# Optimization experiments

Hardware: AMD Instinct MI355X
Metric: run time of the kernel (lower is better)

The kernel has to match this reference:

```python
import jax, jax.numpy as jnp
import numpy as np

N = 50000
NEG_SLOPE = 0.2


def add_self_loops(edge_index, n):
    loop = jnp.arange(n, dtype=edge_index.dtype)
    return jnp.concatenate([edge_index, jnp.stack([loop, loop])], axis=1)


def gatv2_conv(x, edge_index, Wl, bl, Wr, br, att, bias):
    """PyG GATv2Conv (share_weights=False, concat=True, add_self_loops applied by caller).
    x: [N, Fin]; edge_index: [2, E] with row0=src(j), row1=dst(i); att: [H, D].
    Returns (out [N, H*D], alpha [E, H])."""
    src, dst = edge_index[0], edge_index[1]
    H, D = att.shape
    n = x.shape[0]
    xl = (x @ Wl + bl).reshape(n, H, D)   # source-side transform
    xr = (x @ Wr + br).reshape(n, H, D)   # target-side transform
    e = jax.nn.leaky_relu(xl[src] + xr[dst], NEG_SLOPE)        # [E, H, D]
    logit = jnp.einsum('ehd,hd->eh', e, att)                    # [E, H]
    # segment softmax over edges grouped by target node
    lmax = jax.ops.segment_max(logit, dst, num_segments=n)      # [N, H]
    ex = jnp.exp(logit - lmax[dst])
    denom = jax.ops.segment_sum(ex, dst, num_segments=n)
    alpha = ex / denom[dst]                                     # [E, H]
    out = jax.ops.segment_sum(alpha[:, :, None] * xl[src], dst, num_segments=n)  # [N, H, D]
    return out.reshape(n, H * D) + bias, alpha


def setup_inputs() -> dict:
    key = jax.random.key(0)
    ks = jax.random.split(key, 16)
    E = 400000
    x = jax.random.normal(ks[0], (N, 23), dtype=jnp.float32)
    edge_index = jax.random.randint(ks[1], (2, E), 0, N, dtype=jnp.int64)
    H1, D1 = 8, 64
    F1 = H1 * D1  # 512
    s = 0.1
    return {
        'x': x,
        'edge_index': edge_index,
        'Wl1': jax.random.normal(ks[2], (23, F1), dtype=jnp.float32) * s,
        'bl1': jnp.zeros((F1,), jnp.float32),
        'Wr1': jax.random.normal(ks[3], (23, F1), dtype=jnp.float32) * s,
        'br1': jnp.zeros((F1,), jnp.float32),
        'att1': jax.random.normal(ks[4], (H1, D1), dtype=jnp.float32) * s,
        'bias1': jnp.zeros((F1,), jnp.float32),
        'Wl2': jax.random.normal(ks[5], (F1, 1), dtype=jnp.float32) * s,
        'bl2': jnp.zeros((1,), jnp.float32),
        'Wr2': jax.random.normal(ks[6], (F1, 1), dtype=jnp.float32) * s,
        'br2': jnp.zeros((1,), jnp.float32),
        'att2': jax.random.normal(ks[7], (1, 1), dtype=jnp.float32) * s,
        'bias2': jnp.zeros((1,), jnp.float32),
    }


def reference(x, edge_index, Wl1, bl1, Wr1, br1, att1, bias1,
              Wl2, bl2, Wr2, br2, att2, bias2):
    ei = add_self_loops(edge_index, N)
    h, _ = gatv2_conv(x, ei, Wl1, bl1, Wr1, br1, att1, bias1)
    h = jax.nn.relu(h)
    h, alpha = gatv2_conv(h, ei, Wl2, bl2, Wr2, br2, att2, bias2)
    return h, alpha
```

## Files before the change

### kernel.cpp

```cpp
#include <hip/hip_runtime.h>
#include <math.h>

#define NN 50000
#define E0 400000
#define EE 450000
#define FF 512
#define G1 2048
#define NPB ((NN + G1 - 1) / G1)
#define EPB ((EE + G1 - 1) / G1)
#define WAVES_TOTAL (G1 * 4)
#define SCANB 49
#define LOG2E 1.44269504f

__device__ __forceinline__ float leaky(float v) { return fmaxf(v, 0.2f * v); }
__device__ __forceinline__ float blo(unsigned u) { return __uint_as_float(u << 16); }
__device__ __forceinline__ float bhi(unsigned u) { return __uint_as_float(u & 0xffff0000u); }
__device__ __forceinline__ unsigned bpack(float a, float b) {
    unsigned ua = __float_as_uint(a); ua = (ua + 0x7fffu + ((ua >> 16) & 1u)) >> 16;
    unsigned ub = __float_as_uint(b); ub = (ub + 0x7fffu + ((ub >> 16) & 1u)) >> 16;
    return ua | (ub << 16);
}

__global__ __launch_bounds__(256) void k_predeg(
    const float* __restrict__ x,
    const float* __restrict__ Wl1, const float* __restrict__ bl1,
    const float* __restrict__ Wr1, const float* __restrict__ br1,
    const int* __restrict__ ei,
    unsigned* __restrict__ xlb, unsigned* __restrict__ xrb, int* __restrict__ deg)
{
    int b = blockIdx.x, t = threadIdx.x;

    {
        int e = b * EPB + t;
        int e1 = b * EPB + EPB; if (e1 > EE) e1 = EE;
        if (t < EPB && e < e1) {
            int dst = (e < E0) ? ei[E0 + e] : (e - E0);
            atomicAdd(&deg[dst], 1);
        }
    }

    int c0 = 2 * t, c1 = 2 * t + 1;
    float wl0[23], wl1v[23], wr0[23], wr1v[23];
#pragma unroll
    for (int r = 0; r < 23; r++) {
        wl0[r]  = Wl1[r * FF + c0];
        wl1v[r] = Wl1[r * FF + c1];
        wr0[r]  = Wr1[r * FF + c0];
        wr1v[r] = Wr1[r * FF + c1];
    }
    float bl0 = bl1[c0], bl1s = bl1[c1];
    float br0 = br1[c0], br1s = br1[c1];

    int i0 = b * NPB;
    int i1 = i0 + NPB; if (i1 > NN) i1 = NN;
    for (int i = i0; i < i1; i++) {
        int ib = __builtin_amdgcn_readfirstlane(i);
        float a0 = bl0, a1 = bl1s, b0 = br0, b1 = br1s;
#pragma unroll
        for (int r = 0; r < 23; r++) {
            float xv = x[ib * 23 + r];
            a0 += xv * wl0[r];
            a1 += xv * wl1v[r];
            b0 += xv * wr0[r];
            b1 += xv * wr1v[r];
        }
        xlb[(size_t)i * 256 + t] = bpack(a0, a1);
        xrb[(size_t)i * 256 + t] = bpack(b0, b1);
    }
}

__global__ __launch_bounds__(256) void k_scan(
    const int* __restrict__ deg, unsigned* __restrict__ flag,
    int* __restrict__ offs, int* __restrict__ cur)
{
    __shared__ int wsum[4];
    __shared__ int s_prev;
    int b = blockIdx.x, t = threadIdx.x;
    int base = b * 1024 + t * 4;
    int v0 = (base     < NN) ? deg[base]     : 0;
    int v1 = (base + 1 < NN) ? deg[base + 1] : 0;
    int v2 = (base + 2 < NN) ? deg[base + 2] : 0;
    int v3 = (base + 3 < NN) ? deg[base + 3] : 0;
    int tsum = v0 + v1 + v2 + v3;
    int lane = t & 63, wv = t >> 6;
    int sc = tsum;
#pragma unroll
    for (int o = 1; o < 64; o <<= 1) {
        int u = __shfl_up(sc, o, 64);
        if (lane >= o) sc += u;
    }
    if (lane == 63) wsum[wv] = sc;
    __syncthreads();
    int woff = 0;
    for (int k = 0; k < wv; k++) woff += wsum[k];
    int btot = wsum[0] + wsum[1] + wsum[2] + wsum[3];

    if (t == 0) atomicExch(&flag[b], (unsigned)btot + 1u);
    int contrib = 0;
    if (t < b) {
        unsigned f;
        do { f = atomicAdd(&flag[t], 0u); } while (f == 0u);
        contrib = (int)(f - 1u);
    }
    if (t < 64) {
#pragma unroll
        for (int o = 32; o > 0; o >>= 1) contrib += __shfl_xor(contrib, o, 64);
        if (t == 0) s_prev = contrib;
    }
    __syncthreads();
    int add = s_prev;
    int ex = add + woff + sc - tsum;
    if (base     < NN) { offs[base]     = ex;                cur[base]     = ex; }
    if (base + 1 < NN) { offs[base + 1] = ex + v0;           cur[base + 1] = ex + v0; }
    if (base + 2 < NN) { offs[base + 2] = ex + v0 + v1;      cur[base + 2] = ex + v0 + v1; }
    if (base + 3 < NN) { offs[base + 3] = ex + v0 + v1 + v2; cur[base + 3] = ex + v0 + v1 + v2; }
    if (b == SCANB - 1 && t == 255) offs[NN] = add + btot;
}

__global__ void k_scatter(const int* __restrict__ ei, int* __restrict__ cur,
                          int* __restrict__ src_s, int* __restrict__ eid_s)
{
    int e = blockIdx.x * blockDim.x + threadIdx.x;
    if (e >= EE) return;
    int src, dst;
    if (e < E0) { src = ei[e]; dst = ei[E0 + e]; }
    else        { src = e - E0; dst = src; }
    int p = atomicAdd(&cur[dst], 1);
    src_s[p] = src;
    eid_s[p] = e;
}

__global__ __launch_bounds__(256) void k_layer1(
    const uint4* __restrict__ xlb, const uint4* __restrict__ xrb,
    const float* __restrict__ att, const float* __restrict__ bias1,
    const float* __restrict__ Wl2, const float* __restrict__ bl2,
    const float* __restrict__ Wr2, const float* __restrict__ br2,
    const int* __restrict__ offs, const int* __restrict__ src_s,
    float* __restrict__ xl2, float* __restrict__ xr2)
{
    int t = threadIdx.x;
    int l = t & 63;
    int wid = blockIdx.x * 4 + (t >> 6);

    float4 atA = ((const float4*)att)[2 * l];
    float4 atB = ((const float4*)att)[2 * l + 1];
    atA.x *= LOG2E; atA.y *= LOG2E; atA.z *= LOG2E; atA.w *= LOG2E;
    atB.x *= LOG2E; atB.y *= LOG2E; atB.z *= LOG2E; atB.w *= LOG2E;
    float bl2v = bl2[0], br2v = br2[0];

    for (int i = wid; i < NN; i += WAVES_TOTAL) {
        uint4 xq = xrb[(size_t)i * 64 + l];
        float xr0 = blo(xq.x), xr1 = bhi(xq.x), xr2v = blo(xq.y), xr3 = bhi(xq.y);
        float xr4 = blo(xq.z), xr5 = bhi(xq.z), xr6 = blo(xq.w), xr7 = bhi(xq.w);

        float s = 0.f;
        float ac0 = 0.f, ac1 = 0.f, ac2 = 0.f, ac3 = 0.f;
        float ac4 = 0.f, ac5 = 0.f, ac6 = 0.f, ac7 = 0.f;

        int beg = offs[i], deg = offs[i + 1] - beg;

        for (int cb = 0; cb < deg; cb += 64) {
            int cnt = deg - cb; if (cnt > 64) cnt = 64;
            int myj = (l < cnt) ? src_s[beg + cb + l] : 0;

            int j0 = __builtin_amdgcn_readlane(myj, 0);
            uint4 r0 = xlb[(size_t)j0 * 64 + l];
            uint4 r1 = r0, r2 = r0, r3 = r0;
            if (cnt > 1) r1 = xlb[(size_t)__builtin_amdgcn_readlane(myj, 1) * 64 + l];
            if (cnt > 2) r2 = xlb[(size_t)__builtin_amdgcn_readlane(myj, 2) * 64 + l];
            if (cnt > 3) r3 = xlb[(size_t)__builtin_amdgcn_readlane(myj, 3) * 64 + l];

            for (int p = 0; p < cnt; p++) {
                uint4 rn = r0;
                if (p + 4 < cnt)
                    rn = xlb[(size_t)__builtin_amdgcn_readlane(myj, p + 4) * 64 + l];
                float v0 = blo(r0.x), v1 = bhi(r0.x), v2 = blo(r0.y), v3 = bhi(r0.y);
                float v4 = blo(r0.z), v5 = bhi(r0.z), v6 = blo(r0.w), v7 = bhi(r0.w);
                float part;
                part  = atA.x * leaky(v0 + xr0);
                part  = fmaf(atA.y, leaky(v1 + xr1), part);
                part  = fmaf(atA.z, leaky(v2 + xr2v), part);
                part  = fmaf(atA.w, leaky(v3 + xr3), part);
                part  = fmaf(atB.x, leaky(v4 + xr4), part);
                part  = fmaf(atB.y, leaky(v5 + xr5), part);
                part  = fmaf(atB.z, leaky(v6 + xr6), part);
                part  = fmaf(atB.w, leaky(v7 + xr7), part);
                part += __shfl_xor(part, 1, 64);
                part += __shfl_xor(part, 2, 64);
                part += __shfl_xor(part, 4, 64);
                float w = exp2f(part);
                s += w;
                ac0 = fmaf(w, v0, ac0); ac1 = fmaf(w, v1, ac1);
                ac2 = fmaf(w, v2, ac2); ac3 = fmaf(w, v3, ac3);
                ac4 = fmaf(w, v4, ac4); ac5 = fmaf(w, v5, ac5);
                ac6 = fmaf(w, v6, ac6); ac7 = fmaf(w, v7, ac7);
                r0 = r1; r1 = r2; r2 = r3; r3 = rn;
            }
        }

        float inv = 1.f / s;
        float4 bA = ((const float4*)bias1)[2 * l];
        float4 bB = ((const float4*)bias1)[2 * l + 1];
        float h0 = fmaxf(fmaf(ac0, inv, bA.x), 0.f);
        float h1 = fmaxf(fmaf(ac1, inv, bA.y), 0.f);
        float h2 = fmaxf(fmaf(ac2, inv, bA.z), 0.f);
        float h3 = fmaxf(fmaf(ac3, inv, bA.w), 0.f);
        float h4 = fmaxf(fmaf(ac4, inv, bB.x), 0.f);
        float h5 = fmaxf(fmaf(ac5, inv, bB.y), 0.f);
        float h6 = fmaxf(fmaf(ac6, inv, bB.z), 0.f);
        float h7 = fmaxf(fmaf(ac7, inv, bB.w), 0.f);

        float4 wlA = ((const float4*)Wl2)[2 * l];
        float4 wlB = ((const float4*)Wl2)[2 * l + 1];
        float4 wrA = ((const float4*)Wr2)[2 * l];
        float4 wrB = ((const float4*)Wr2)[2 * l + 1];
        float pl = h0 * wlA.x + h1 * wlA.y + h2 * wlA.z + h3 * wlA.w
                 + h4 * wlB.x + h5 * wlB.y + h6 * wlB.z + h7 * wlB.w;
        float pr = h0 * wrA.x + h1 * wrA.y + h2 * wrA.z + h3 * wrA.w
                 + h4 * wrB.x + h5 * wrB.y + h6 * wrB.z + h7 * wrB.w;
#pragma unroll
        for (int o = 32; o > 0; o >>= 1) {
            pl += __shfl_xor(pl, o, 64);
            pr += __shfl_xor(pr, o, 64);
        }
        if (l == 0) {
            xl2[i] = pl + bl2v;
            xr2[i] = pr + br2v;
        }
    }
}

__global__ void k_layer2(const float* __restrict__ xl2, const float* __restrict__ xr2,
                         const float* __restrict__ att2, const float* __restrict__ bias2,
                         const int* __restrict__ offs, const int* __restrict__ src_s,
                         const int* __restrict__ eid_s, float* __restrict__ out)
{
    int i = blockIdx.x * blockDim.x + threadIdx.x;
    if (i >= NN) return;
    int beg = offs[i], end = offs[i + 1];
    float xri = xr2[i];
    float a2l = att2[0] * LOG2E;
    float s = 0.f, num = 0.f;
    for (int p = beg; p < end; p++) {
        float v = xl2[src_s[p]];
        float w = exp2f(leaky(v + xri) * a2l);
        s += w;
        num = fmaf(w, v, num);
    }
    out[i] = num / s + bias2[0];
    float inv = 1.f / s;
    for (int p = beg; p < end; p++) {
        float v = xl2[src_s[p]];
        float w = exp2f(leaky(v + xri) * a2l);
        out[NN + eid_s[p]] = w * inv;
    }
}

extern "C" void kernel_launch(void* const* d_in, const int* in_sizes, int n_in,
                              void* d_out, int out_size, void* d_ws, size_t ws_size,
                              hipStream_t stream)
{
    const float* x     = (const float*)d_in[0];
    const int*   ei    = (const int*)d_in[1];
    const float* Wl1   = (const float*)d_in[2];
    const float* bl1   = (const float*)d_in[3];
    const float* Wr1   = (const float*)d_in[4];
    const float* br1   = (const float*)d_in[5];
    const float* att1  = (const float*)d_in[6];
    const float* bias1 = (const float*)d_in[7];
    const float* Wl2   = (const float*)d_in[8];
    const float* bl2   = (const float*)d_in[9];
    const float* Wr2   = (const float*)d_in[10];
    const float* br2   = (const float*)d_in[11];
    const float* att2  = (const float*)d_in[12];
    const float* bias2 = (const float*)d_in[13];
    float* out = (float*)d_out;

    char* ws = (char*)d_ws;
    unsigned* xlb = (unsigned*)ws; ws += (size_t)NN * 256 * 4;
    unsigned* xrb = (unsigned*)ws; ws += (size_t)NN * 256 * 4;
    float* xl2  = (float*)ws;      ws += (size_t)NN * 4;
    float* xr2  = (float*)ws;      ws += (size_t)NN * 4;
    int* deg    = (int*)ws;        ws += (size_t)NN * 4;
    unsigned* flag = (unsigned*)ws; ws += (size_t)64 * 4;
    int* offs   = (int*)ws;        ws += (size_t)(NN + 1) * 4;
    int* cur    = (int*)ws;        ws += (size_t)NN * 4;
    int* src_s  = (int*)ws;        ws += (size_t)EE * 4;
    int* eid_s  = (int*)ws;        ws += (size_t)EE * 4;

    hipMemsetAsync(deg, 0, (size_t)(NN + 64) * 4, stream);

    k_predeg<<<G1, 256, 0, stream>>>(x, Wl1, bl1, Wr1, br1, ei, xlb, xrb, deg);
    k_scan<<<SCANB, 256, 0, stream>>>(deg, flag, offs, cur);
    k_scatter<<<(EE + 255) / 256, 256, 0, stream>>>(ei, cur, src_s, eid_s);
    k_layer1<<<G1, 256, 0, stream>>>((const uint4*)xlb, (const uint4*)xrb,
                                     att1, bias1, Wl2, bl2, Wr2, br2,
                                     offs, src_s, xl2, xr2);
    k_layer2<<<(NN + 255) / 256, 256, 0, stream>>>(xl2, xr2, att2, bias2,
                                                   offs, src_s, eid_s, out);
}
```

Baseline: 258.9 us.

## Switch layer-1 features to fp16 with packed dot2 attention and accumulation

Stores the layer-1 source and target features as fp16 instead of bf16. The edge loop now uses packed half adds, rewrites leaky ReLU as 0.6*t + 0.4*|t| so the attention logit becomes fdot2 instructions, and accumulates the weighted sum in packed fp16. It also stages x rows in shared memory in the projection kernel and cuts the gather prefetch depth from 4 to 2. The aim is fewer VALU instructions per edge, with the risk of fp16 overflow or accuracy loss in the accumulators and less latency hiding on the gathers.

```diff
diff --git a/kernel.cpp b/kernel.cpp
--- a/kernel.cpp
+++ b/kernel.cpp
@@ -12,32 +12,34 @@
 #define SCANB 49
 #define LOG2E 1.44269504f
 
+typedef _Float16 h2 __attribute__((ext_vector_type(2)));
+
+__device__ __forceinline__ h2 uas_h2(unsigned u) { union { unsigned u; h2 h; } c; c.u = u; return c.h; }
+__device__ __forceinline__ unsigned h2as_u(h2 h) { union { unsigned u; h2 h; } c; c.h = h; return c.u; }
 __device__ __forceinline__ float leaky(float v) { return fmaxf(v, 0.2f * v); }
-__device__ __forceinline__ float blo(unsigned u) { return __uint_as_float(u << 16); }
-__device__ __forceinline__ float bhi(unsigned u) { return __uint_as_float(u & 0xffff0000u); }
-__device__ __forceinline__ unsigned bpack(float a, float b) {
-    unsigned ua = __float_as_uint(a); ua = (ua + 0x7fffu + ((ua >> 16) & 1u)) >> 16;
-    unsigned ub = __float_as_uint(b); ub = (ub + 0x7fffu + ((ub >> 16) & 1u)) >> 16;
-    return ua | (ub << 16);
-}
 
 __global__ __launch_bounds__(256) void k_predeg(
     const float* __restrict__ x,
     const float* __restrict__ Wl1, const float* __restrict__ bl1,
     const float* __restrict__ Wr1, const float* __restrict__ br1,
     const int* __restrict__ ei,
-    unsigned* __restrict__ xlb, unsigned* __restrict__ xrb, int* __restrict__ deg)
-{
+    unsigned* __restrict__ xlh, unsigned* __restrict__ xrh, int* __restrict__ deg)
+{
+    __shared__ float sx[NPB * 23];
     int b = blockIdx.x, t = threadIdx.x;
+    int i0 = b * NPB;
+    int i1 = i0 + NPB; if (i1 > NN) i1 = NN;
+    int nf = (i1 - i0) * 23;
 
     {
         int e = b * EPB + t;
-        int e1 = b * EPB + EPB; if (e1 > EE) e1 = EE;
-        if (t < EPB && e < e1) {
+        if (t < EPB && e < EE) {
             int dst = (e < E0) ? ei[E0 + e] : (e - E0);
             atomicAdd(&deg[dst], 1);
         }
     }
+
+    for (int k = t; k < nf; k += 256) sx[k] = x[i0 * 23 + k];
 
     int c0 = 2 * t, c1 = 2 * t + 1;
     float wl0[23], wl1v[23], wr0[23], wr1v[23];
@@ -50,22 +52,22 @@
     }
     float bl0 = bl1[c0], bl1s = bl1[c1];
     float br0 = br1[c0], br1s = br1[c1];
-
-    int i0 = b * NPB;
-    int i1 = i0 + NPB; if (i1 > NN) i1 = NN;
-    for (int i = i0; i < i1; i++) {
-        int ib = __builtin_amdgcn_readfirstlane(i);
-        float a0 = bl0, a1 = bl1s, b0 = br0, b1 = br1s;
+    __syncthreads();
+
+    for (int n = 0; n < i1 - i0; n++) {
+        float a0 = bl0, a1 = bl1s, b0v = br0, b1v = br1s;
 #pragma unroll
         for (int r = 0; r < 23; r++) {
-            float xv = x[ib * 23 + r];
-            a0 += xv * wl0[r];
-            a1 += xv * wl1v[r];
-            b0 += xv * wr0[r];
-            b1 += xv * wr1v[r];
-        }
-        xlb[(size_t)i * 256 + t] = bpack(a0, a1);
-        xrb[(size_t)i * 256 + t] = bpack(b0, b1);
+            float xv = sx[n * 23 + r];
+            a0  += xv * wl0[r];
+            a1  += xv * wl1v[r];
+            b0v += xv * wr0[r];
+            b1v += xv * wr1v[r];
+        }
+        h2 hl = { (_Float16)a0,  (_Float16)a1  };
+        h2 hr = { (_Float16)b0v, (_Float16)b1v };
+        xlh[(size_t)(i0 + n) * 256 + t] = h2as_u(hl);
+        xrh[(size_t)(i0 + n) * 256 + t] = h2as_u(hr);
     }
 }
 
@@ -131,7 +133,7 @@
 }
 
 __global__ __launch_bounds__(256) void k_layer1(
-    const uint4* __restrict__ xlb, const uint4* __restrict__ xrb,
+    const uint4* __restrict__ xlh, const uint4* __restrict__ xrh,
     const float* __restrict__ att, const float* __restrict__ bias1,
     const float* __restrict__ Wl2, const float* __restrict__ bl2,
     const float* __restrict__ Wr2, const float* __restrict__ br2,
@@ -144,18 +146,22 @@
 
     float4 atA = ((const float4*)att)[2 * l];
     float4 atB = ((const float4*)att)[2 * l + 1];
-    atA.x *= LOG2E; atA.y *= LOG2E; atA.z *= LOG2E; atA.w *= LOG2E;
-    atB.x *= LOG2E; atB.y *= LOG2E; atB.z *= LOG2E; atB.w *= LOG2E;
+    h2 a6_0 = { (_Float16)(0.6f * LOG2E * atA.x), (_Float16)(0.6f * LOG2E * atA.y) };
+    h2 a6_1 = { (_Float16)(0.6f * LOG2E * atA.z), (_Float16)(0.6f * LOG2E * atA.w) };
+    h2 a6_2 = { (_Float16)(0.6f * LOG2E * atB.x), (_Float16)(0.6f * LOG2E * atB.y) };
+    h2 a6_3 = { (_Float16)(0.6f * LOG2E * atB.z), (_Float16)(0.6f * LOG2E * atB.w) };
+    h2 a4_0 = { (_Float16)(0.4f * LOG2E * atA.x), (_Float16)(0.4f * LOG2E * atA.y) };
+    h2 a4_1 = { (_Float16)(0.4f * LOG2E * atA.z), (_Float16)(0.4f * LOG2E * atA.w) };
+    h2 a4_2 = { (_Float16)(0.4f * LOG2E * atB.x), (_Float16)(0.4f * LOG2E * atB.y) };
+    h2 a4_3 = { (_Float16)(0.4f * LOG2E * atB.z), (_Float16)(0.4f * LOG2E * atB.w) };
     float bl2v = bl2[0], br2v = br2[0];
 
     for (int i = wid; i < NN; i += WAVES_TOTAL) {
-        uint4 xq = xrb[(size_t)i * 64 + l];
-        float xr0 = blo(xq.x), xr1 = bhi(xq.x), xr2v = blo(xq.y), xr3 = bhi(xq.y);
-        float xr4 = blo(xq.z), xr5 = bhi(xq.z), xr6 = blo(xq.w), xr7 = bhi(xq.w);
+        uint4 xq = xrh[(size_t)i * 64 + l];
+        h2 q0 = uas_h2(xq.x), q1 = uas_h2(xq.y), q2 = uas_h2(xq.z), q3 = uas_h2(xq.w);
 
         float s = 0.f;
-        float ac0 = 0.f, ac1 = 0.f, ac2 = 0.f, ac3 = 0.f;
-        float ac4 = 0.f, ac5 = 0.f, ac6 = 0.f, ac7 = 0.f;
+        h2 A0 = { 0, 0 }, A1 = { 0, 0 }, A2 = { 0, 0 }, A3 = { 0, 0 };
 
         int beg = offs[i], deg = offs[i + 1] - beg;
 
@@ -164,59 +170,64 @@
             int myj = (l < cnt) ? src_s[beg + cb + l] : 0;
 
             int j0 = __builtin_amdgcn_readlane(myj, 0);
-            uint4 r0 = xlb[(size_t)j0 * 64 + l];
-            uint4 r1 = r0, r2 = r0, r3 = r0;
-            if (cnt > 1) r1 = xlb[(size_t)__builtin_amdgcn_readlane(myj, 1) * 64 + l];
-            if (cnt > 2) r2 = xlb[(size_t)__builtin_amdgcn_readlane(myj, 2) * 64 + l];
-            if (cnt > 3) r3 = xlb[(size_t)__builtin_amdgcn_readlane(myj, 3) * 64 + l];
+            uint4 r0 = xlh[(size_t)j0 * 64 + l];
+            uint4 r1 = r0;
+            if (cnt > 1) r1 = xlh[(size_t)__builtin_amdgcn_readlane(myj, 1) * 64 + l];
 
             for (int p = 0; p < cnt; p++) {
                 uint4 rn = r0;
-                if (p + 4 < cnt)
-                    rn = xlb[(size_t)__builtin_amdgcn_readlane(myj, p + 4) * 64 + l];
-                float v0 = blo(r0.x), v1 = bhi(r0.x), v2 = blo(r0.y), v3 = bhi(r0.y);
-                float v4 = blo(r0.z), v5 = bhi(r0.z), v6 = blo(r0.w), v7 = bhi(r0.w);
-                float part;
-                part  = atA.x * leaky(v0 + xr0);
-                part  = fmaf(atA.y, leaky(v1 + xr1), part);
-                part  = fmaf(atA.z, leaky(v2 + xr2v), part);
-                part  = fmaf(atA.w, leaky(v3 + xr3), part);
-                part  = fmaf(atB.x, leaky(v4 + xr4), part);
-                part  = fmaf(atB.y, leaky(v5 + xr5), part);
-                part  = fmaf(atB.z, leaky(v6 + xr6), part);
-                part  = fmaf(atB.w, leaky(v7 + xr7), part);
+                if (p + 2 < cnt)
+                    rn = xlh[(size_t)__builtin_amdgcn_readlane(myj, p + 2) * 64 + l];
+
+                h2 p0 = uas_h2(r0.x), p1 = uas_h2(r0.y), p2 = uas_h2(r0.z), p3 = uas_h2(r0.w);
+                h2 t0 = p0 + q0, t1 = p1 + q1, t2 = p2 + q2, t3 = p3 + q3;
+                h2 b0 = uas_h2(h2as_u(t0) & 0x7fff7fffu);
+                h2 b1 = uas_h2(h2as_u(t1) & 0x7fff7fffu);
+                h2 b2 = uas_h2(h2as_u(t2) & 0x7fff7fffu);
+                h2 b3 = uas_h2(h2as_u(t3) & 0x7fff7fffu);
+                float part = 0.f;
+                part = __builtin_amdgcn_fdot2(a6_0, t0, part, false);
+                part = __builtin_amdgcn_fdot2(a4_0, b0, part, false);
+                part = __builtin_amdgcn_fdot2(a6_1, t1, part, false);
+                part = __builtin_amdgcn_fdot2(a4_1, b1, part, false);
+                part = __builtin_amdgcn_fdot2(a6_2, t2, part, false);
+                part = __builtin_amdgcn_fdot2(a4_2, b2, part, false);
+                part = __builtin_amdgcn_fdot2(a6_3, t3, part, false);
+                part = __builtin_amdgcn_fdot2(a4_3, b3, part, false);
                 part += __shfl_xor(part, 1, 64);
                 part += __shfl_xor(part, 2, 64);
                 part += __shfl_xor(part, 4, 64);
                 float w = exp2f(part);
                 s += w;
-                ac0 = fmaf(w, v0, ac0); ac1 = fmaf(w, v1, ac1);
-                ac2 = fmaf(w, v2, ac2); ac3 = fmaf(w, v3, ac3);
-                ac4 = fmaf(w, v4, ac4); ac5 = fmaf(w, v5, ac5);
-                ac6 = fmaf(w, v6, ac6); ac7 = fmaf(w, v7, ac7);
-                r0 = r1; r1 = r2; r2 = r3; r3 = rn;
+                _Float16 wh = (_Float16)w;
+                h2 w2 = { wh, wh };
+                A0 += w2 * p0;
+                A1 += w2 * p1;
+                A2 += w2 * p2;
+                A3 += w2 * p3;
+                r0 = r1; r1 = rn;
             }
         }
 
         float inv = 1.f / s;
         float4 bA = ((const float4*)bias1)[2 * l];
         float4 bB = ((const float4*)bias1)[2 * l + 1];
-        float h0 = fmaxf(fmaf(ac0, inv, bA.x), 0.f);
-        float h1 = fmaxf(fmaf(ac1, inv, bA.y), 0.f);
-        float h2 = fmaxf(fmaf(ac2, inv, bA.z), 0.f);
-        float h3 = fmaxf(fmaf(ac3, inv, bA.w), 0.f);
-        float h4 = fmaxf(fmaf(ac4, inv, bB.x), 0.f);
-        float h5 = fmaxf(fmaf(ac5, inv, bB.y), 0.f);
-        float h6 = fmaxf(fmaf(ac6, inv, bB.z), 0.f);
-        float h7 = fmaxf(fmaf(ac7, inv, bB.w), 0.f);
+        float h0 = fmaxf(fmaf((float)A0[0], inv, bA.x), 0.f);
+        float h1 = fmaxf(fmaf((float)A0[1], inv, bA.y), 0.f);
+        float h2v = fmaxf(fmaf((float)A1[0], inv, bA.z), 0.f);
+        float h3 = fmaxf(fmaf((float)A1[1], inv, bA.w), 0.f);
+        float h4 = fmaxf(fmaf((float)A2[0], inv, bB.x), 0.f);
+        float h5 = fmaxf(fmaf((float)A2[1], inv, bB.y), 0.f);
+        float h6 = fmaxf(fmaf((float)A3[0], inv, bB.z), 0.f);
+        float h7 = fmaxf(fmaf((float)A3[1], inv, bB.w), 0.f);
 
         float4 wlA = ((const float4*)Wl2)[2 * l];
         float4 wlB = ((const float4*)Wl2)[2 * l + 1];
         float4 wrA = ((const float4*)Wr2)[2 * l];
         float4 wrB = ((const float4*)Wr2)[2 * l + 1];
-        float pl = h0 * wlA.x + h1 * wlA.y + h2 * wlA.z + h3 * wlA.w
+        float pl = h0 * wlA.x + h1 * wlA.y + h2v * wlA.z + h3 * wlA.w
                  + h4 * wlB.x + h5 * wlB.y + h6 * wlB.z + h7 * wlB.w;
-        float pr = h0 * wrA.x + h1 * wrA.y + h2 * wrA.z + h3 * wrA.w
+        float pr = h0 * wrA.x + h1 * wrA.y + h2v * wrA.z + h3 * wrA.w
                  + h4 * wrB.x + h5 * wrB.y + h6 * wrB.z + h7 * wrB.w;
 #pragma unroll
         for (int o = 32; o > 0; o >>= 1) {
@@ -277,8 +288,8 @@
     float* out = (float*)d_out;
 
     char* ws = (char*)d_ws;
-    unsigned* xlb = (unsigned*)ws; ws += (size_t)NN * 256 * 4;
-    unsigned* xrb = (unsigned*)ws; ws += (size_t)NN * 256 * 4;
+    unsigned* xlh = (unsigned*)ws; ws += (size_t)NN * 256 * 4;
+    unsigned* xrh = (unsigned*)ws; ws += (size_t)NN * 256 * 4;
     float* xl2  = (float*)ws;      ws += (size_t)NN * 4;
     float* xr2  = (float*)ws;      ws += (size_t)NN * 4;
     int* deg    = (int*)ws;        ws += (size_t)NN * 4;
@@ -290,10 +301,10 @@
 
     hipMemsetAsync(deg, 0, (size_t)(NN + 64) * 4, stream);
 
-    k_predeg<<<G1, 256, 0, stream>>>(x, Wl1, bl1, Wr1, br1, ei, xlb, xrb, deg);
+    k_predeg<<<G1, 256, 0, stream>>>(x, Wl1, bl1, Wr1, br1, ei, xlh, xrh, deg);
     k_scan<<<SCANB, 256, 0, stream>>>(deg, flag, offs, cur);
     k_scatter<<<(EE + 255) / 256, 256, 0, stream>>>(ei, cur, src_s, eid_s);
-    k_layer1<<<G1, 256, 0, stream>>>((const uint4*)xlb, (const uint4*)xrb,
+    k_layer1<<<G1, 256, 0, stream>>>((const uint4*)xlh, (const uint4*)xrh,
                                      att1, bias1, Wl2, bl2, Wr2, br2,
                                      offs, src_s, xl2, xr2);
     k_layer2<<<(NN + 255) / 256, 256, 0, stream>>>(xl2, xr2, att2, bias2,
```

New measurement: 252.4 us. 1.03x faster.
